# Performance work log

Hardware: AMD Instinct MI355X
Metric: run time of the kernel (lower is better)

The kernel has to match this reference:

```python
import jax, jax.numpy as jnp
import numpy as np

N = 50000      # nodes
R = 4          # relations
E = 1600000    # edges per relation
IN = 256       # in_feats
H = 256        # h_feats
C = 16         # num_classes


def setup_inputs() -> dict:
    key = jax.random.key(0)
    ks = jax.random.split(key, 8)
    X = jax.random.normal(ks[0], (N, IN), jnp.float32)
    edge_index = jax.random.randint(ks[1], (R, 2, E), 0, N, dtype=jnp.int32)
    W1 = jax.random.normal(ks[2], (R, IN, H), jnp.float32) * (1.0 / np.sqrt(IN))
    W2 = jax.random.normal(ks[3], (R, H, H), jnp.float32) * (1.0 / np.sqrt(H))
    att_q = jax.random.normal(ks[4], (H,), jnp.float32) * (1.0 / np.sqrt(H))
    tau = jnp.asarray(2.0, jnp.float32)
    W_out = jax.random.normal(ks[5], (H, C), jnp.float32) * (1.0 / np.sqrt(H))
    b_out = jnp.zeros((C,), jnp.float32)
    return {"X": X, "edge_index": edge_index, "W1": W1, "W2": W2,
            "att_q": att_q, "tau": tau, "W_out": W_out, "b_out": b_out}


def _sym_norm_spmm(edge, feat):
    """out = D^{-1/2} A D^{-1/2} @ feat for one relation, edge: [2,E]."""
    row, col = edge[0], edge[1]
    ones = jnp.ones(edge.shape[1], feat.dtype)
    deg_r = jax.ops.segment_sum(ones, row, num_segments=N)
    deg_c = jax.ops.segment_sum(ones, col, num_segments=N)
    dinv_r = jax.lax.rsqrt(jnp.maximum(deg_r, 1.0))
    dinv_c = jax.lax.rsqrt(jnp.maximum(deg_c, 1.0))
    w = dinv_r[row] * dinv_c[col]                      # [E]
    msg = w[:, None] * feat[col]                       # gather + scale
    return jax.ops.segment_sum(msg, row, num_segments=N)  # [N, F]


def _rel_layer(edge_index, feat, W):
    # vmapped over relations: ReLU(A_r feat W_r) -> [R, N, H]
    def one(edge, Wr):
        return jax.nn.relu(_sym_norm_spmm(edge, feat) @ Wr)
    return jax.vmap(one)(edge_index, W)


def reference(X, edge_index, W1, W2, att_q, tau, W_out, b_out):
    # Layer 1: mean over relations (eval mode: no dropout)
    H1 = _rel_layer(edge_index, X, W1)        # [R, N, H]
    h1 = H1.mean(axis=0)                      # [N, H]
    # Layer 2 with relation attention
    H2 = _rel_layer(edge_index, h1, W2)       # [R, N, H]
    scores = jnp.einsum('rnh,h->nr', H2, att_q)
    tau_c = jnp.clip(tau, 0.5, 5.0)
    alpha = jax.nn.softmax(scores / tau_c, axis=1)   # [N, R]
    h2_att = jnp.einsum('nr,rnh->nh', alpha, H2)
    h2 = H2.mean(axis=0) + h2_att             # residual fusion
    logits = h2 @ W_out + b_out               # [N, C]
    return logits, alpha
```

## Files before the change

kernel.cpp:

```cpp
#include <hip/hip_runtime.h>
#include <hip/hip_bf16.h>
#include <stdint.h>

#define NODES 50000
#define RELS  4
#define EDGES 1600000
#define FEAT  256
#define NCLS  16
#define MPAD  50048
#define RPS   50016
#define SCHUNK 1024
#define NSBLK  49
#define NCHUNK 64
#define CHUNKE 25000
#define NB     782

typedef __attribute__((ext_vector_type(8))) short short8;
typedef __attribute__((ext_vector_type(8))) unsigned short u16x8;
typedef __attribute__((ext_vector_type(4))) float f32x4;

static __device__ __forceinline__ float bf2f(unsigned short u) {
    return __uint_as_float(((unsigned int)u) << 16);
}
static __device__ __forceinline__ unsigned short f2bf(float f) {
    unsigned int x = __float_as_uint(f);
    unsigned int r = x + 0x7fffu + ((x >> 16) & 1u);
    return (unsigned short)(r >> 16);
}


__global__ __launch_bounds__(256)
void k_bhist(const int* __restrict__ edges, int arr_off, unsigned* __restrict__ part) {
    int chunk = blockIdx.x, rel = blockIdx.y, t = threadIdx.x;
    const int* arr = edges + (size_t)rel * 2 * EDGES + arr_off + (size_t)chunk * CHUNKE;
    __shared__ unsigned h[NB];
    for (int i = t; i < NB; i += 256) h[i] = 0;
    __syncthreads();
    for (int e = t; e < CHUNKE; e += 256) atomicAdd(&h[((unsigned)arr[e]) >> 6], 1u);
    __syncthreads();
    unsigned* po = part + ((size_t)rel * NCHUNK + chunk) * NB;
    for (int i = t; i < NB; i += 256) po[i] = h[i];
}

__global__ __launch_bounds__(256)
void k_bscan(const unsigned* __restrict__ part, unsigned* __restrict__ off,
             unsigned* __restrict__ bbase) {
    int rel = blockIdx.x, t = threadIdx.x;
    const int BPT = 4;
    int b0 = t * BPT;
    unsigned s = 0;
#pragma unroll
    for (int j = 0; j < BPT; ++j) {
        int b = b0 + j;
        unsigned x = 0;
        if (b < NB)
            for (int c = 0; c < NCHUNK; ++c)
                x += part[((size_t)rel * NCHUNK + c) * NB + b];
        s += x;
    }
    __shared__ unsigned sh[256];
    sh[t] = s;
    __syncthreads();
    for (int o = 1; o < 256; o <<= 1) {
        unsigned u = (t >= o) ? sh[t - o] : 0;
        __syncthreads();
        sh[t] += u;
        __syncthreads();
    }
    unsigned base = sh[t] - s;
#pragma unroll
    for (int j = 0; j < BPT; ++j) {
        int b = b0 + j;
        if (b < NB) {
            bbase[rel * (NB + 1) + b] = base;
            unsigned acc = base;
            for (int c = 0; c < NCHUNK; ++c) {
                size_t o2 = ((size_t)rel * NCHUNK + c) * NB + b;
                off[o2] = acc;
                acc += part[o2];
            }
            base = acc;
        }
    }
    if (t == 255) bbase[rel * (NB + 1) + NB] = sh[255];
}

__global__ __launch_bounds__(256)
void k_scatR(const int* __restrict__ edges, const unsigned* __restrict__ off,
             int2* __restrict__ ebuf) {
    int chunk = blockIdx.x, rel = blockIdx.y, t = threadIdx.x;
    const int* rows = edges + (size_t)rel * 2 * EDGES + (size_t)chunk * CHUNKE;
    const int* cols = rows + EDGES;
    __shared__ unsigned cur[NB];
    const unsigned* po = off + ((size_t)rel * NCHUNK + chunk) * NB;
    for (int i = t; i < NB; i += 256) cur[i] = po[i];
    __syncthreads();
    int2* eb = ebuf + (size_t)rel * EDGES;
    for (int e = t; e < CHUNKE; e += 256) {
        int r = rows[e], c = cols[e];
        unsigned pos = atomicAdd(&cur[((unsigned)r) >> 6], 1u);
        eb[pos] = make_int2(r, c);
    }
}

__global__ __launch_bounds__(256)
void k_scatC(const int* __restrict__ edges, const unsigned* __restrict__ off,
             int* __restrict__ cbuf) {
    int chunk = blockIdx.x, rel = blockIdx.y, t = threadIdx.x;
    const int* cols = edges + (size_t)rel * 2 * EDGES + EDGES + (size_t)chunk * CHUNKE;
    __shared__ unsigned cur[NB];
    const unsigned* po = off + ((size_t)rel * NCHUNK + chunk) * NB;
    for (int i = t; i < NB; i += 256) cur[i] = po[i];
    __syncthreads();
    int* cb = cbuf + (size_t)rel * EDGES;
    for (int e = t; e < CHUNKE; e += 256) {
        int c = cols[e];
        unsigned pos = atomicAdd(&cur[((unsigned)c) >> 6], 1u);
        cb[pos] = c;
    }
}

__global__ __launch_bounds__(256)
void k_countR(const int2* __restrict__ ebuf, const unsigned* __restrict__ bbase,
              int* __restrict__ deg_row) {
    int b = blockIdx.x, rel = blockIdx.y, t = threadIdx.x;
    unsigned s = bbase[rel * (NB + 1) + b], e = bbase[rel * (NB + 1) + b + 1];
    __shared__ unsigned cnt[64];
    if (t < 64) cnt[t] = 0;
    __syncthreads();
    const int2* eb = ebuf + (size_t)rel * EDGES;
    for (unsigned i = s + t; i < e; i += 256) atomicAdd(&cnt[eb[i].x & 63], 1u);
    __syncthreads();
    int base = b * 64;
    if (t < 64 && base + t < NODES) deg_row[(size_t)rel * NODES + base + t] = (int)cnt[t];
}

__global__ __launch_bounds__(256)
void k_countC(const int* __restrict__ cbuf, const unsigned* __restrict__ bbase,
              int* __restrict__ deg_col) {
    int b = blockIdx.x, rel = blockIdx.y, t = threadIdx.x;
    unsigned s = bbase[rel * (NB + 1) + b], e = bbase[rel * (NB + 1) + b + 1];
    __shared__ unsigned cnt[64];
    if (t < 64) cnt[t] = 0;
    __syncthreads();
    const int* cb = cbuf + (size_t)rel * EDGES;
    for (unsigned i = s + t; i < e; i += 256) atomicAdd(&cnt[cb[i] & 63], 1u);
    __syncthreads();
    int base = b * 64;
    if (t < 64 && base + t < NODES) deg_col[(size_t)rel * NODES + base + t] = (int)cnt[t];
}

__global__ void k_dinv(const int* __restrict__ deg_row, const int* __restrict__ deg_col,
                       float* dinv_row, float* dinv_col) {
    int idx = blockIdx.x * blockDim.x + threadIdx.x;
    if (idx >= RELS * NODES) return;
    int dr = deg_row[idx]; if (dr < 1) dr = 1;
    int dc = deg_col[idx]; if (dc < 1) dc = 1;
    dinv_row[idx] = rsqrtf((float)dr);
    dinv_col[idx] = rsqrtf((float)dc);
}

__global__ __launch_bounds__(256)
void k_scanA(const int* __restrict__ deg, int* __restrict__ tmp, int* __restrict__ btot) {
    int r = blockIdx.y, blk = blockIdx.x, t = threadIdx.x;
    int i0 = blk * SCHUNK + t * 4;
    const int* d = deg + (size_t)r * NODES;
    int4 v = make_int4(0, 0, 0, 0);
    if (i0 + 3 < NODES) v = *(const int4*)(d + i0);
    else if (i0 < NODES) {
        v.x = d[i0];
        if (i0 + 1 < NODES) v.y = d[i0 + 1];
        if (i0 + 2 < NODES) v.z = d[i0 + 2];
    }
    int s = v.x + v.y + v.z + v.w;
    __shared__ int sh[256];
    sh[t] = s;
    __syncthreads();
    for (int off = 1; off < 256; off <<= 1) {
        int u = (t >= off) ? sh[t - off] : 0;
        __syncthreads();
        sh[t] += u;
        __syncthreads();
    }
    int excl = sh[t] - s;
    int4 o;
    o.x = excl; o.y = excl + v.x; o.z = o.y + v.y; o.w = o.z + v.z;
    int* tp = tmp + (size_t)r * NODES;
    if (i0 + 3 < NODES) *(int4*)(tp + i0) = o;
    else if (i0 < NODES) {
        tp[i0] = o.x;
        if (i0 + 1 < NODES) tp[i0 + 1] = o.y;
        if (i0 + 2 < NODES) tp[i0 + 2] = o.z;
    }
    if (t == 255) btot[r * 64 + blk] = sh[255];
}

__global__ void k_scanB(int* __restrict__ btot, int* __restrict__ row_ptr) {
    int r = blockIdx.x;
    if (threadIdx.x != 0) return;
    int acc = 0;
    for (int b = 0; b < NSBLK; ++b) {
        int v = btot[r * 64 + b];
        btot[r * 64 + b] = acc;
        acc += v;
    }
    row_ptr[r * RPS + NODES] = acc;
}

__global__ __launch_bounds__(256)
void k_scanC(const int* __restrict__ tmp, const int* __restrict__ btot,
             int* __restrict__ row_ptr) {
    int r = blockIdx.y, blk = blockIdx.x, t = threadIdx.x;
    int i0 = blk * SCHUNK + t * 4;
    int off = btot[r * 64 + blk];
    const int* tp = tmp + (size_t)r * NODES;
    int* rp = row_ptr + (size_t)r * RPS;
    if (i0 + 3 < NODES) {
        int4 v = *(const int4*)(tp + i0);
        rp[i0] = v.x + off; rp[i0 + 1] = v.y + off;
        rp[i0 + 2] = v.z + off; rp[i0 + 3] = v.w + off;
    } else if (i0 < NODES) {
        for (int j = 0; j < 4 && i0 + j < NODES; ++j)
            rp[i0 + j] = tp[i0 + j] + off;
    }
}

__global__ __launch_bounds__(256)
void k_place(const int2* __restrict__ ebuf, const unsigned* __restrict__ bbase,
             const int* __restrict__ row_ptr, int* __restrict__ csr_col) {
    int b = blockIdx.x, rel = blockIdx.y, t = threadIdx.x;
    unsigned s = bbase[rel * (NB + 1) + b], e = bbase[rel * (NB + 1) + b + 1];
    __shared__ int cur[64];
    int base = b * 64;
    const int* rp = row_ptr + (size_t)rel * RPS;
    if (t < 64) cur[t] = (base + t < NODES) ? rp[base + t] : 0;
    __syncthreads();
    const int2* eb = ebuf + (size_t)rel * EDGES;
    int* cc = csr_col + (size_t)rel * EDGES;
    for (unsigned i = s + t; i < e; i += 256) {
        int2 ec = eb[i];
        int pos = atomicAdd(&cur[ec.x - base], 1);
        cc[pos] = ec.y;
    }
}


__global__ void k_f2bf(const float* __restrict__ src, unsigned short* __restrict__ dst, int count) {
    int i = blockIdx.x * blockDim.x + threadIdx.x;
    if (i < count) dst[i] = f2bf(src[i]);
}

__global__ void k_wt(const float* __restrict__ W, unsigned short* __restrict__ Wt) {
    int idx = blockIdx.x * blockDim.x + threadIdx.x;
    if (idx >= RELS * FEAT * FEAT) return;
    int r = idx >> 16;
    int rem = idx & 65535;
    int n = rem >> 8;
    int k = rem & 255;
    Wt[idx] = f2bf(W[(size_t)r * FEAT * FEAT + (size_t)k * FEAT + n]);
}


__global__ __launch_bounds__(256)
void k_spmm(const unsigned short* __restrict__ feat, const int* __restrict__ row_ptr,
            const int* __restrict__ csr_col, const float* __restrict__ dinv_row,
            const float* __restrict__ dinv_col, unsigned short* __restrict__ aggbf, int rel) {
    int wave = (blockIdx.x * blockDim.x + threadIdx.x) >> 6;
    int lane = threadIdx.x & 63;
    if (wave >= NODES) return;
    int row = wave;
    int half = lane >> 5;
    int l32  = lane & 31;
    int start = row_ptr[rel * RPS + row];
    int end   = row_ptr[rel * RPS + row + 1];
    const int* cols = csr_col + (size_t)rel * EDGES;
    const float* dc = dinv_col + rel * NODES;
    const unsigned short* fb = feat + l32 * 8;
    float acc[8] = {0.f, 0.f, 0.f, 0.f, 0.f, 0.f, 0.f, 0.f};
    int j = start + half;
    for (; j + 2 < end; j += 4) {
        int c0 = cols[j];
        int c1 = cols[j + 2];
        float w0 = dc[c0];
        float w1 = dc[c1];
        u16x8 u0 = *(const u16x8*)(fb + (size_t)c0 * FEAT);
        u16x8 u1 = *(const u16x8*)(fb + (size_t)c1 * FEAT);
#pragma unroll
        for (int i = 0; i < 8; ++i) acc[i] += w0 * bf2f(u0[i]);
#pragma unroll
        for (int i = 0; i < 8; ++i) acc[i] += w1 * bf2f(u1[i]);
    }
    if (j < end) {
        int c0 = cols[j];
        float w0 = dc[c0];
        u16x8 u0 = *(const u16x8*)(fb + (size_t)c0 * FEAT);
#pragma unroll
        for (int i = 0; i < 8; ++i) acc[i] += w0 * bf2f(u0[i]);
    }
#pragma unroll
    for (int i = 0; i < 8; ++i) acc[i] += __shfl_down(acc[i], 32, 64);
    if (half == 0) {
        float dr = dinv_row[rel * NODES + row];
        u16x8 o;
#pragma unroll
        for (int i = 0; i < 8; ++i) o[i] = f2bf(acc[i] * dr);
        *(u16x8*)(aggbf + (size_t)row * FEAT + l32 * 8) = o;
    }
}


__global__ __launch_bounds__(256)
void k_gemm1(const unsigned short* __restrict__ Abase, const unsigned short* __restrict__ Wt,
             unsigned short* __restrict__ h1bf) {
    __shared__ __align__(16) unsigned short As[128 * 64];
    __shared__ __align__(16) unsigned short Bs[128 * 64];
    int tid = threadIdx.x;
    int wave = tid >> 6, lane = tid & 63;
    int quad = lane >> 4, l16 = lane & 15;
    int wm = (wave & 1) * 64, wn = (wave >> 1) * 64;
    int row0 = blockIdx.x * 128, n0 = blockIdx.y * 128;

    f32x4 hacc[4][4];
#pragma unroll
    for (int mi = 0; mi < 4; ++mi)
#pragma unroll
        for (int ni = 0; ni < 4; ++ni)
            hacc[mi][ni] = (f32x4){0.f, 0.f, 0.f, 0.f};

    for (int r = 0; r < RELS; ++r) {
        const unsigned short* A  = Abase + (size_t)r * MPAD * FEAT;
        const unsigned short* Bt = Wt + (size_t)r * FEAT * FEAT;
        f32x4 acc[4][4];
#pragma unroll
        for (int mi = 0; mi < 4; ++mi)
#pragma unroll
            for (int ni = 0; ni < 4; ++ni)
                acc[mi][ni] = (f32x4){0.f, 0.f, 0.f, 0.f};

        for (int k0 = 0; k0 < FEAT; k0 += 64) {
#pragma unroll
            for (int issue = 0; issue < 4; ++issue) {
                int flat = issue * 256 + tid;
                int row = flat >> 3;
                int gr = flat & 7;
                int sg = gr ^ (row & 7);
                *(uint4*)&As[flat * 8] = *(const uint4*)(A + (size_t)(row0 + row) * FEAT + k0 + sg * 8);
                *(uint4*)&Bs[flat * 8] = *(const uint4*)(Bt + (size_t)(n0 + row) * FEAT + k0 + sg * 8);
            }
            __syncthreads();
#pragma unroll
            for (int ks = 0; ks < 2; ++ks) {
                int g = ks * 4 + quad;
                short8 af[4], bfr[4];
#pragma unroll
                for (int mi = 0; mi < 4; ++mi) {
                    int m = wm + mi * 16 + l16;
                    af[mi] = *(const short8*)&As[m * 64 + ((g ^ (m & 7)) << 3)];
                }
#pragma unroll
                for (int ni = 0; ni < 4; ++ni) {
                    int n = wn + ni * 16 + l16;
                    bfr[ni] = *(const short8*)&Bs[n * 64 + ((g ^ (n & 7)) << 3)];
                }
#pragma unroll
                for (int mi = 0; mi < 4; ++mi)
#pragma unroll
                    for (int ni = 0; ni < 4; ++ni)
                        acc[mi][ni] = __builtin_amdgcn_mfma_f32_16x16x32_bf16(af[mi], bfr[ni], acc[mi][ni], 0, 0, 0);
            }
            __syncthreads();
        }
#pragma unroll
        for (int mi = 0; mi < 4; ++mi)
#pragma unroll
            for (int ni = 0; ni < 4; ++ni)
#pragma unroll
                for (int i = 0; i < 4; ++i) {
                    float v = acc[mi][ni][i];
                    hacc[mi][ni][i] += 0.25f * (v > 0.f ? v : 0.f);
                }
    }

#pragma unroll
    for (int mi = 0; mi < 4; ++mi)
#pragma unroll
        for (int ni = 0; ni < 4; ++ni) {
            int col = n0 + wn + ni * 16 + l16;
#pragma unroll
            for (int i = 0; i < 4; ++i) {
                int row = row0 + wm + mi * 16 + quad * 4 + i;
                if (row < NODES) h1bf[(size_t)row * FEAT + col] = f2bf(hacc[mi][ni][i]);
            }
        }
}

__global__ __launch_bounds__(256)
void k_gemm2(const unsigned short* __restrict__ A, const unsigned short* __restrict__ Bt,
             unsigned short* __restrict__ H2) {
    __shared__ __align__(16) unsigned short As[128 * 64];
    __shared__ __align__(16) unsigned short Bs[128 * 64];
    int tid = threadIdx.x;
    int wave = tid >> 6, lane = tid & 63;
    int quad = lane >> 4, l16 = lane & 15;
    int wm = (wave & 1) * 64, wn = (wave >> 1) * 64;
    int row0 = blockIdx.x * 128, n0 = blockIdx.y * 128;

    f32x4 acc[4][4];
#pragma unroll
    for (int mi = 0; mi < 4; ++mi)
#pragma unroll
        for (int ni = 0; ni < 4; ++ni)
            acc[mi][ni] = (f32x4){0.f, 0.f, 0.f, 0.f};

    for (int k0 = 0; k0 < FEAT; k0 += 64) {
#pragma unroll
        for (int issue = 0; issue < 4; ++issue) {
            int flat = issue * 256 + tid;
            int row = flat >> 3;
            int gr = flat & 7;
            int sg = gr ^ (row & 7);
            *(uint4*)&As[flat * 8] = *(const uint4*)(A + (size_t)(row0 + row) * FEAT + k0 + sg * 8);
            *(uint4*)&Bs[flat * 8] = *(const uint4*)(Bt + (size_t)(n0 + row) * FEAT + k0 + sg * 8);
        }
        __syncthreads();
#pragma unroll
        for (int ks = 0; ks < 2; ++ks) {
            int g = ks * 4 + quad;
            short8 af[4], bfr[4];
#pragma unroll
            for (int mi = 0; mi < 4; ++mi) {
                int m = wm + mi * 16 + l16;
                af[mi] = *(const short8*)&As[m * 64 + ((g ^ (m & 7)) << 3)];
            }
#pragma unroll
            for (int ni = 0; ni < 4; ++ni) {
                int n = wn + ni * 16 + l16;
                bfr[ni] = *(const short8*)&Bs[n * 64 + ((g ^ (n & 7)) << 3)];
            }
#pragma unroll
            for (int mi = 0; mi < 4; ++mi)
#pragma unroll
                for (int ni = 0; ni < 4; ++ni)
                    acc[mi][ni] = __builtin_amdgcn_mfma_f32_16x16x32_bf16(af[mi], bfr[ni], acc[mi][ni], 0, 0, 0);
        }
        __syncthreads();
    }

#pragma unroll
    for (int mi = 0; mi < 4; ++mi)
#pragma unroll
        for (int ni = 0; ni < 4; ++ni) {
            int col = n0 + wn + ni * 16 + l16;
#pragma unroll
            for (int i = 0; i < 4; ++i) {
                int row = row0 + wm + mi * 16 + quad * 4 + i;
                if (row < NODES) {
                    float v = acc[mi][ni][i];
                    H2[(size_t)row * FEAT + col] = f2bf(v > 0.f ? v : 0.f);
                }
            }
        }
}


__global__ __launch_bounds__(256)
void k_scores(const unsigned short* __restrict__ H2bf, const float* __restrict__ att_q,
              const float* __restrict__ tau_p, float* __restrict__ alpha_out) {
    int wave = (blockIdx.x * blockDim.x + threadIdx.x) >> 6;
    int lane = threadIdx.x & 63;
    if (wave >= NODES) return;
    int n = wave;
    float4 q = *(const float4*)(att_q + lane * 4);
    float s[RELS];
#pragma unroll
    for (int r = 0; r < RELS; ++r) {
        ushort4 u = *(const ushort4*)(H2bf + ((size_t)r * NODES + n) * FEAT + lane * 4);
        s[r] = bf2f(u.x) * q.x + bf2f(u.y) * q.y + bf2f(u.z) * q.z + bf2f(u.w) * q.w;
    }
#pragma unroll
    for (int off = 32; off > 0; off >>= 1) {
#pragma unroll
        for (int r = 0; r < RELS; ++r) s[r] += __shfl_down(s[r], off, 64);
    }
    if (lane == 0) {
        float tau = tau_p[0];
        tau = fminf(fmaxf(tau, 0.5f), 5.0f);
        float it = 1.0f / tau;
        float m = fmaxf(fmaxf(s[0], s[1]), fmaxf(s[2], s[3]));
        float e0 = expf((s[0] - m) * it);
        float e1 = expf((s[1] - m) * it);
        float e2 = expf((s[2] - m) * it);
        float e3 = expf((s[3] - m) * it);
        float inv = 1.0f / (e0 + e1 + e2 + e3);
        float4 al = { e0 * inv, e1 * inv, e2 * inv, e3 * inv };
        *(float4*)(alpha_out + (size_t)n * 4) = al;
    }
}


__global__ __launch_bounds__(256)
void k_logits(const unsigned short* __restrict__ H2bf, const float* __restrict__ alpha,
              const float* __restrict__ W_out, const float* __restrict__ b_out,
              float* __restrict__ logits) {
    int gid = blockIdx.x * blockDim.x + threadIdx.x;
    if (gid >= NODES * NCLS) return;
    int n = gid >> 4;
    int c = gid & 15;
    float a0 = 0.25f + alpha[(size_t)n * 4 + 0];
    float a1 = 0.25f + alpha[(size_t)n * 4 + 1];
    float a2 = 0.25f + alpha[(size_t)n * 4 + 2];
    float a3 = 0.25f + alpha[(size_t)n * 4 + 3];
    const unsigned short* h0 = H2bf + (size_t)n * FEAT;
    const size_t rs = (size_t)NODES * FEAT;
    float acc = b_out[c];
#pragma unroll 4
    for (int h = 0; h < FEAT; ++h) {
        float h2 = a0 * bf2f(h0[h]) + a1 * bf2f(h0[h + rs]) +
                   a2 * bf2f(h0[h + 2 * rs]) + a3 * bf2f(h0[h + 3 * rs]);
        acc += h2 * W_out[h * NCLS + c];
    }
    logits[gid] = acc;
}


static inline int cdiv(int a, int b) { return (a + b - 1) / b; }

extern "C" void kernel_launch(void* const* d_in, const int* in_sizes, int n_in,
                              void* d_out, int out_size, void* d_ws, size_t ws_size,
                              hipStream_t stream) {
    const float* X     = (const float*)d_in[0];
    const int*   edges = (const int*)d_in[1];
    const float* W1    = (const float*)d_in[2];
    const float* W2    = (const float*)d_in[3];
    const float* att_q = (const float*)d_in[4];
    const float* tau   = (const float*)d_in[5];
    const float* W_out = (const float*)d_in[6];
    const float* b_out = (const float*)d_in[7];

    float* logits = (float*)d_out;
    float* alpha  = logits + (size_t)NODES * NCLS;

    char* p = (char*)d_ws;
    auto carve = [&](size_t bytes) -> char* {
        char* q = p;
        p += (bytes + 255) & ~(size_t)255;
        return q;
    };
    int*   deg_row  = (int*)carve((size_t)RELS * NODES * 4);
    int*   deg_col  = (int*)carve((size_t)RELS * NODES * 4);
    float* dinv_row = (float*)carve((size_t)RELS * NODES * 4);
    float* dinv_col = (float*)carve((size_t)RELS * NODES * 4);
    int*   row_ptr  = (int*)carve((size_t)RELS * RPS * 4 + 256);
    int*   tmp      = (int*)carve((size_t)RELS * NODES * 4);
    int*   btot     = (int*)carve((size_t)RELS * 64 * 4);
    int*   csr_col  = (int*)carve((size_t)RELS * EDGES * 4);
    unsigned short* Xbf  = (unsigned short*)carve((size_t)NODES * FEAT * 2);
    unsigned short* h1bf = (unsigned short*)carve((size_t)NODES * FEAT * 2);
    unsigned short* W1t  = (unsigned short*)carve((size_t)RELS * FEAT * FEAT * 2);
    unsigned short* W2t  = (unsigned short*)carve((size_t)RELS * FEAT * FEAT * 2);
    const size_t AGGS = (size_t)MPAD * FEAT * 2;
    char* BIG = carve(AGGS + (size_t)RELS * NODES * FEAT * 2);
    int2*     ebuf = (int2*)BIG;
    int*      cbuf = (int*)(BIG + (size_t)RELS * EDGES * 8);
    char*     q = BIG + (size_t)RELS * EDGES * 12;
    unsigned* partR = (unsigned*)q;               q += (size_t)RELS * NCHUNK * NB * 4;
    unsigned* offR  = (unsigned*)q;               q += (size_t)RELS * NCHUNK * NB * 4;
    unsigned* partC = (unsigned*)q;               q += (size_t)RELS * NCHUNK * NB * 4;
    unsigned* offC  = (unsigned*)q;               q += (size_t)RELS * NCHUNK * NB * 4;
    unsigned* bbR   = (unsigned*)q;               q += (size_t)RELS * (NB + 1) * 4;
    unsigned* bbC   = (unsigned*)q;
    unsigned short* aggbf = (unsigned short*)BIG;
    unsigned short* H2bf  = (unsigned short*)(BIG + AGGS);

    {
        dim3 hg(NCHUNK, RELS);
        dim3 bg(NB, RELS);
        k_bhist<<<hg, 256, 0, stream>>>(edges, 0, partR);
        k_bhist<<<hg, 256, 0, stream>>>(edges, EDGES, partC);
        k_bscan<<<RELS, 256, 0, stream>>>(partR, offR, bbR);
        k_bscan<<<RELS, 256, 0, stream>>>(partC, offC, bbC);
        k_scatR<<<hg, 256, 0, stream>>>(edges, offR, ebuf);
        k_scatC<<<hg, 256, 0, stream>>>(edges, offC, cbuf);
        k_countR<<<bg, 256, 0, stream>>>(ebuf, bbR, deg_row);
        k_countC<<<bg, 256, 0, stream>>>(cbuf, bbC, deg_col);
        k_dinv<<<cdiv(RELS * NODES, 256), 256, 0, stream>>>(deg_row, deg_col, dinv_row, dinv_col);
        dim3 sg(NSBLK, RELS);
        k_scanA<<<sg, 256, 0, stream>>>(deg_row, tmp, btot);
        k_scanB<<<RELS, 64, 0, stream>>>(btot, row_ptr);
        k_scanC<<<sg, 256, 0, stream>>>(tmp, btot, row_ptr);
        k_place<<<bg, 256, 0, stream>>>(ebuf, bbR, row_ptr, csr_col);
    }

    k_f2bf<<<cdiv(NODES * FEAT, 256), 256, 0, stream>>>(X, Xbf, NODES * FEAT);
    k_wt<<<cdiv(RELS * FEAT * FEAT, 256), 256, 0, stream>>>(W1, W1t);
    k_wt<<<cdiv(RELS * FEAT * FEAT, 256), 256, 0, stream>>>(W2, W2t);

    dim3 gemm_grid(MPAD / 128, FEAT / 128);

    for (int r = 0; r < RELS; ++r)
        k_spmm<<<cdiv(NODES * 64, 256), 256, 0, stream>>>(Xbf, row_ptr, csr_col,
                                                          dinv_row, dinv_col,
                                                          aggbf + (size_t)r * MPAD * FEAT, r);
    k_gemm1<<<gemm_grid, 256, 0, stream>>>(aggbf, W1t, h1bf);

    for (int r = 0; r < RELS; ++r) {
        k_spmm<<<cdiv(NODES * 64, 256), 256, 0, stream>>>(h1bf, row_ptr, csr_col,
                                                          dinv_row, dinv_col, aggbf, r);
        k_gemm2<<<gemm_grid, 256, 0, stream>>>(aggbf, W2t + (size_t)r * FEAT * FEAT,
                                               H2bf + (size_t)r * NODES * FEAT);
    }

    k_scores<<<cdiv(NODES * 64, 256), 256, 0, stream>>>(H2bf, att_q, tau, alpha);
    k_logits<<<cdiv(NODES * NCLS, 256), 256, 0, stream>>>(H2bf, alpha, W_out, b_out, logits);
}
```

Measured before the change: 1.634 ms.

## Fuse attention scores and output projection into one persistent wave-per-node kernel

Replaces the separate scores and logits kernels with one persistent kernel. Each wave handles one node at a time: it computes the relation scores, the softmax, the fused h2 combination and the 16-class projection. W_out is held in registers and partial sums are reduced through LDS. This removes the old logits kernel, which reread the four H2 rows per class with poor coalescing, and it prefetches the next node's rows. The LDS reduction relies on intra-wave ordering with a manual waitcnt instead of a barrier, and it adds register pressure.

Result: faster. 1.523 ms (-6.7%).

```diff
diff --git a/kernel.cpp b/kernel.cpp
--- a/kernel.cpp
+++ b/kernel.cpp
@@ -464,62 +464,105 @@
 
 
 __global__ __launch_bounds__(256)
-void k_scores(const unsigned short* __restrict__ H2bf, const float* __restrict__ att_q,
-              const float* __restrict__ tau_p, float* __restrict__ alpha_out) {
-    int wave = (blockIdx.x * blockDim.x + threadIdx.x) >> 6;
-    int lane = threadIdx.x & 63;
-    if (wave >= NODES) return;
-    int n = wave;
+void k_attn_out(const unsigned short* __restrict__ H2bf, const float* __restrict__ att_q,
+                const float* __restrict__ tau_p, const float* __restrict__ W_out,
+                const float* __restrict__ b_out, float* __restrict__ alpha_out,
+                float* __restrict__ logits) {
+    __shared__ float red[4][64 * 17];
+    int tid = threadIdx.x;
+    int wid = tid >> 6;
+    int lane = tid & 63;
+    int gwave = blockIdx.x * 4 + wid;
+    int nwaves = gridDim.x * 4;
+
     float4 q = *(const float4*)(att_q + lane * 4);
-    float s[RELS];
-#pragma unroll
-    for (int r = 0; r < RELS; ++r) {
-        ushort4 u = *(const ushort4*)(H2bf + ((size_t)r * NODES + n) * FEAT + lane * 4);
-        s[r] = bf2f(u.x) * q.x + bf2f(u.y) * q.y + bf2f(u.z) * q.z + bf2f(u.w) * q.w;
-    }
-#pragma unroll
-    for (int off = 32; off > 0; off >>= 1) {
-#pragma unroll
-        for (int r = 0; r < RELS; ++r) s[r] += __shfl_down(s[r], off, 64);
-    }
-    if (lane == 0) {
-        float tau = tau_p[0];
-        tau = fminf(fmaxf(tau, 0.5f), 5.0f);
-        float it = 1.0f / tau;
+    float tau = fminf(fmaxf(tau_p[0], 0.5f), 5.0f);
+    float itau = 1.0f / tau;
+    f32x4 Wr[4][4];
+#pragma unroll
+    for (int j = 0; j < 4; ++j)
+#pragma unroll
+        for (int c4 = 0; c4 < 4; ++c4) {
+            float4 w = *(const float4*)(W_out + (size_t)(lane * 4 + j) * NCLS + c4 * 4);
+            Wr[j][c4] = (f32x4){w.x, w.y, w.z, w.w};
+        }
+    float bc = b_out[lane & 15];
+    float* myred = &red[wid][0];
+    int cls = lane & 15;
+    int rb = (lane >> 4) * 16;
+
+    int n = gwave;
+    if (n >= NODES) return;
+    ushort4 u[RELS];
+#pragma unroll
+    for (int r = 0; r < RELS; ++r)
+        u[r] = *(const ushort4*)(H2bf + ((size_t)r * NODES + n) * FEAT + lane * 4);
+
+    while (n < NODES) {
+        int nn = n + nwaves;
+        int nc = (nn < NODES) ? nn : n;
+        ushort4 un[RELS];
+#pragma unroll
+        for (int r = 0; r < RELS; ++r)
+            un[r] = *(const ushort4*)(H2bf + ((size_t)r * NODES + nc) * FEAT + lane * 4);
+
+        float h[RELS][4];
+#pragma unroll
+        for (int r = 0; r < RELS; ++r) {
+            h[r][0] = bf2f(u[r].x); h[r][1] = bf2f(u[r].y);
+            h[r][2] = bf2f(u[r].z); h[r][3] = bf2f(u[r].w);
+        }
+        float s[RELS];
+#pragma unroll
+        for (int r = 0; r < RELS; ++r)
+            s[r] = h[r][0] * q.x + h[r][1] * q.y + h[r][2] * q.z + h[r][3] * q.w;
+#pragma unroll
+        for (int off = 1; off < 64; off <<= 1) {
+#pragma unroll
+            for (int r = 0; r < RELS; ++r) s[r] += __shfl_xor(s[r], off, 64);
+        }
         float m = fmaxf(fmaxf(s[0], s[1]), fmaxf(s[2], s[3]));
-        float e0 = expf((s[0] - m) * it);
-        float e1 = expf((s[1] - m) * it);
-        float e2 = expf((s[2] - m) * it);
-        float e3 = expf((s[3] - m) * it);
-        float inv = 1.0f / (e0 + e1 + e2 + e3);
-        float4 al = { e0 * inv, e1 * inv, e2 * inv, e3 * inv };
-        *(float4*)(alpha_out + (size_t)n * 4) = al;
-    }
-}
-
-
-__global__ __launch_bounds__(256)
-void k_logits(const unsigned short* __restrict__ H2bf, const float* __restrict__ alpha,
-              const float* __restrict__ W_out, const float* __restrict__ b_out,
-              float* __restrict__ logits) {
-    int gid = blockIdx.x * blockDim.x + threadIdx.x;
-    if (gid >= NODES * NCLS) return;
-    int n = gid >> 4;
-    int c = gid & 15;
-    float a0 = 0.25f + alpha[(size_t)n * 4 + 0];
-    float a1 = 0.25f + alpha[(size_t)n * 4 + 1];
-    float a2 = 0.25f + alpha[(size_t)n * 4 + 2];
-    float a3 = 0.25f + alpha[(size_t)n * 4 + 3];
-    const unsigned short* h0 = H2bf + (size_t)n * FEAT;
-    const size_t rs = (size_t)NODES * FEAT;
-    float acc = b_out[c];
-#pragma unroll 4
-    for (int h = 0; h < FEAT; ++h) {
-        float h2 = a0 * bf2f(h0[h]) + a1 * bf2f(h0[h + rs]) +
-                   a2 * bf2f(h0[h + 2 * rs]) + a3 * bf2f(h0[h + 3 * rs]);
-        acc += h2 * W_out[h * NCLS + c];
-    }
-    logits[gid] = acc;
+        float e[RELS];
+        float esum = 0.f;
+#pragma unroll
+        for (int r = 0; r < RELS; ++r) { e[r] = expf((s[r] - m) * itau); esum += e[r]; }
+        float inv = 1.0f / esum;
+        float a[RELS];
+#pragma unroll
+        for (int r = 0; r < RELS; ++r) a[r] = e[r] * inv;
+        if (lane == 0)
+            *(float4*)(alpha_out + (size_t)n * 4) = make_float4(a[0], a[1], a[2], a[3]);
+
+        float w0 = 0.25f + a[0], w1 = 0.25f + a[1], w2 = 0.25f + a[2], w3 = 0.25f + a[3];
+        float h2[4];
+#pragma unroll
+        for (int j = 0; j < 4; ++j)
+            h2[j] = w0 * h[0][j] + w1 * h[1][j] + w2 * h[2][j] + w3 * h[3][j];
+
+        f32x4 acc[4];
+#pragma unroll
+        for (int c4 = 0; c4 < 4; ++c4)
+            acc[c4] = h2[0] * Wr[0][c4] + h2[1] * Wr[1][c4]
+                    + h2[2] * Wr[2][c4] + h2[3] * Wr[3][c4];
+
+#pragma unroll
+        for (int c4 = 0; c4 < 4; ++c4)
+#pragma unroll
+            for (int i = 0; i < 4; ++i)
+                myred[lane * 17 + c4 * 4 + i] = acc[c4][i];
+        asm volatile("s_waitcnt lgkmcnt(0)" ::: "memory");
+        float t = 0.f;
+#pragma unroll
+        for (int k = 0; k < 16; ++k) t += myred[(rb + k) * 17 + cls];
+        t += __shfl_xor(t, 16, 64);
+        t += __shfl_xor(t, 32, 64);
+        if (lane < 16) logits[(size_t)n * NCLS + lane] = t + bc;
+        asm volatile("" ::: "memory");
+
+#pragma unroll
+        for (int r = 0; r < RELS; ++r) u[r] = un[r];
+        n = nn;
+    }
 }
 
 
@@ -610,6 +653,5 @@
                                                H2bf + (size_t)r * NODES * FEAT);
     }
 
-    k_scores<<<cdiv(NODES * 64, 256), 256, 0, stream>>>(H2bf, att_q, tau, alpha);
-    k_logits<<<cdiv(NODES * NCLS, 256), 256, 0, stream>>>(H2bf, alpha, W_out, b_out, logits);
-}
+    k_attn_out<<<1024, 256, 0, stream>>>(H2bf, att_q, tau, W_out, b_out, alpha, logits);
+}
```
